# Kernel tuning notes

Hardware: AMD Instinct MI355X
Metric: run time of the kernel (lower is better)

## Reference

```python
import jax, jax.numpy as jnp
import numpy as np

COMMITMENT_COST = 0.25

def _conv(x, w, stride, pad):
    return jax.lax.conv_general_dilated(
        x, w, window_strides=(stride, stride),
        padding=((pad, pad), (pad, pad)),
        dimension_numbers=("NCHW", "OIHW", "NCHW"))

def _gelu(x):
    return jax.nn.gelu(x, approximate=False)

def setup_inputs() -> dict:
    key = jax.random.key(0)
    ks = jax.random.split(key, 9)
    def w(k, shape):
        fan_in = shape[1] * shape[2] * shape[3]
        return jax.random.normal(k, shape, jnp.float32) / jnp.sqrt(fan_in)
    return {
        "x": jax.random.normal(ks[0], (32, 3, 256, 256), jnp.float32),
        "enc_w1": w(ks[1], (64, 3, 5, 5)),
        "enc_w2": w(ks[2], (64, 64, 5, 5)),
        "enc_w3": w(ks[3], (64, 64, 2, 2)),
        "dec_w1": w(ks[4], (512, 64, 2, 2)),
        "dec_w2": w(ks[5], (256, 512, 2, 2)),
        "dec_w3": w(ks[6], (256, 256, 2, 2)),
        "codes": jax.random.normal(ks[7], (24, 64), jnp.float32),
        "ema_count": jax.random.uniform(ks[8], (24,), jnp.float32) + 0.1,
    }

def reference(x, enc_w1, enc_w2, enc_w3, dec_w1, dec_w2, dec_w3, codes, ema_count):
    # ---- encoder: 256 -> 128 -> 64 -> 63, channels 3 -> 64 ----
    z = _conv(x, enc_w1, 2, 2)
    z = _gelu(z)
    z = _conv(z, enc_w2, 2, 2)
    z = _gelu(z)
    z = _conv(z, enc_w3, 1, 0)          # [B, 64, 63, 63]

    # ---- VQ codebook (EMA variant: commitment loss only) ----
    B, C, H, W = z.shape
    zf = jnp.transpose(z, (0, 2, 3, 1)).reshape(-1, C)          # [N, C]
    # squared L2 distances to each code
    d = (jnp.sum(zf * zf, axis=1, keepdims=True)
         - 2.0 * zf @ codes.T
         + jnp.sum(codes * codes, axis=1))                       # [N, K]
    idx = jnp.argmin(d, axis=1)                                  # [N]
    zq = codes[idx].reshape(B, H, W, C).transpose(0, 3, 1, 2)    # [B, C, H, W]

    vq_loss = COMMITMENT_COST * jnp.mean(
        (jax.lax.stop_gradient(zq) - z) ** 2)
    # straight-through estimator
    z_hat = z + jax.lax.stop_gradient(zq - z)

    # code probabilities from EMA cluster counts, gathered per position
    probs = ema_count / jnp.sum(ema_count)                       # [K]
    z_probs = probs[idx].reshape(B, H, W)                        # [B, H, W]

    # ---- decoder: 63 -> 64 -> 63 -> 64, channels 64 -> 512 -> 256 -> 256 ----
    y = _conv(z_hat, dec_w1, 1, 1)
    y = _gelu(y)
    y = _conv(y, dec_w2, 1, 0)
    y = _gelu(y)
    x_hat = _conv(y, dec_w3, 1, 1)      # [B, 256, 64, 64]

    return (x_hat, z_probs, vq_loss)
```

## Files before the change

kernel.cpp:

```cpp
#include <hip/hip_runtime.h>
#include <hip/hip_bf16.h>


#define DEV_INLINE __device__ __forceinline__

typedef __attribute__((ext_vector_type(8))) short bf16x8;
typedef __attribute__((ext_vector_type(4))) float f32x4;

#define GLL16(g, l) __builtin_amdgcn_global_load_lds(                      \
    (const __attribute__((address_space(1))) void*)(g),                    \
    (__attribute__((address_space(3))) void*)(l), 16, 0, 0)

DEV_INLINE float gelu_exact(float v) {
    return 0.5f * v * (1.0f + erff(v * 0.70710678118654752440f));
}

__global__ void wtf_k(const float* __restrict__ w, float* __restrict__ wt,
                      int C, int total) {
    int t = blockIdx.x * 256 + threadIdx.x;
    if (t >= total) return;
    int oc = t & 63;
    int rest = t >> 6;
    int tap = rest % 25, c = rest / 25;
    wt[t] = w[(oc * C + c) * 25 + tap];
}

template<int C, int IH, int IW>
__global__ __launch_bounds__(256) void conv5s2_t(
    const float* __restrict__ xg,
    const float* __restrict__ wt,
    float* __restrict__ outg) {
    constexpr int OH = IH / 2, OW = IW / 2;
    __shared__ float xin[35 * 36];
    __shared__ float wl[1600];
    const int tid = threadIdx.x;
    const int n = blockIdx.z;
    const int OY0 = blockIdx.y * 16, OX0 = blockIdx.x * 16;
    const int IY0 = OY0 * 2 - 2, IX0 = OX0 * 2 - 2;
    const int og = tid & 3;
    const int pg = tid >> 2;
    const int py = (pg >> 3) * 2, px = (pg & 7) * 2;
    const int ry = py * 2, rx = px * 2;

    f32x4 a00 = {0,0,0,0}, a01 = a00, a02 = a00, a03 = a00;
    f32x4 a10 = a00, a11 = a00, a12 = a00, a13 = a00;
    f32x4 a20 = a00, a21 = a00, a22 = a00, a23 = a00;
    f32x4 a30 = a00, a31 = a00, a32 = a00, a33 = a00;

    const float* xn = xg + (size_t)n * C * IH * IW;
    for (int c = 0; c < C; ++c) {
        {
            const float4* wsrc = (const float4*)(wt + c * 1600);
            float4* wdst = (float4*)wl;
            wdst[tid] = wsrc[tid];
            if (tid < 144) wdst[256 + tid] = wsrc[256 + tid];
        }
        const float* zc = xn + (size_t)c * IH * IW;
        for (int i = tid; i < 1225; i += 256) {
            int r = i / 35, cl = i - r * 35;
            int iy = IY0 + r, ix = IX0 + cl;
            float v = 0.f;
            if ((unsigned)iy < (unsigned)IH && (unsigned)ix < (unsigned)IW)
                v = zc[(size_t)iy * IW + ix];
            xin[r * 36 + cl] = v;
        }
        __syncthreads();
#pragma unroll
        for (int ky = 0; ky < 5; ++ky) {
            const float* r0 = xin + (ry + ky) * 36 + rx;
            const float* r1 = r0 + 72;
#pragma unroll
            for (int kx = 0; kx < 5; ++kx) {
                const f32x4* wq = (const f32x4*)(wl + (ky * 5 + kx) * 64 + og * 16);
                f32x4 w0 = wq[0], w1 = wq[1], w2 = wq[2], w3 = wq[3];
                float xA = r0[kx], xB = r0[kx + 2];
                float xC = r1[kx], xD = r1[kx + 2];
                a00 += xA * w0; a01 += xA * w1; a02 += xA * w2; a03 += xA * w3;
                a10 += xB * w0; a11 += xB * w1; a12 += xB * w2; a13 += xB * w3;
                a20 += xC * w0; a21 += xC * w1; a22 += xC * w2; a23 += xC * w3;
                a30 += xD * w0; a31 += xD * w1; a32 += xD * w2; a33 += xD * w3;
            }
        }
        __syncthreads();
    }
    const int ocb = og * 16;
#define CSTORE(v, oy, ox, q) {                                                \
        float* o = outg + (((size_t)n * 64 + ocb + (q) * 4) * OH + (oy)) * OW \
                   + (ox);                                                    \
        o[0]               = gelu_exact((v).x);                               \
        o[(size_t)OH * OW]     = gelu_exact((v).y);                           \
        o[(size_t)2 * OH * OW] = gelu_exact((v).z);                           \
        o[(size_t)3 * OH * OW] = gelu_exact((v).w); }
    CSTORE(a00, OY0 + py,     OX0 + px,     0); CSTORE(a01, OY0 + py,     OX0 + px,     1);
    CSTORE(a02, OY0 + py,     OX0 + px,     2); CSTORE(a03, OY0 + py,     OX0 + px,     3);
    CSTORE(a10, OY0 + py,     OX0 + px + 1, 0); CSTORE(a11, OY0 + py,     OX0 + px + 1, 1);
    CSTORE(a12, OY0 + py,     OX0 + px + 1, 2); CSTORE(a13, OY0 + py,     OX0 + px + 1, 3);
    CSTORE(a20, OY0 + py + 1, OX0 + px,     0); CSTORE(a21, OY0 + py + 1, OX0 + px,     1);
    CSTORE(a22, OY0 + py + 1, OX0 + px,     2); CSTORE(a23, OY0 + py + 1, OX0 + px,     3);
    CSTORE(a30, OY0 + py + 1, OX0 + px + 1, 0); CSTORE(a31, OY0 + py + 1, OX0 + px + 1, 1);
    CSTORE(a32, OY0 + py + 1, OX0 + px + 1, 2); CSTORE(a33, OY0 + py + 1, OX0 + px + 1, 3);
#undef CSTORE
}

__global__ void conv3_k(const float* __restrict__ z2,
                        const float* __restrict__ w,
                        float* __restrict__ z) {
    __shared__ float wl[1024];
    const int oc0 = blockIdx.y * 4;
    for (int i = threadIdx.x; i < 1024; i += 256) {
        int j = i & 3, r = i >> 2;
        wl[i] = w[(oc0 + j) * 256 + r];
    }
    __syncthreads();
    const int s = blockIdx.x * 256 + threadIdx.x;
    if (s >= 3969) return;
    const int n = blockIdx.z;
    const int oy = s / 63, ox = s % 63;
    const float4* wv = (const float4*)wl;
    float a0 = 0.f, a1 = 0.f, a2 = 0.f, a3 = 0.f;
    const float* zn = z2 + n * 64 * 4096;
    for (int c = 0; c < 64; ++c) {
        const float* zc = zn + c * 4096;
#pragma unroll
        for (int tap = 0; tap < 4; ++tap) {
            int iy = oy + (tap >> 1), ix = ox + (tap & 1);
            float xv = zc[iy * 64 + ix];
            float4 wq = wv[c * 4 + tap];
            a0 += xv * wq.x; a1 += xv * wq.y; a2 += xv * wq.z; a3 += xv * wq.w;
        }
    }
    int obase = (n * 64 + oc0) * 3969 + s;
    z[obase]            = a0;
    z[obase + 3969]     = a1;
    z[obase + 2 * 3969] = a2;
    z[obase + 3 * 3969] = a3;
}

__global__ void vq_k(const float* __restrict__ z,
                     const float* __restrict__ codes,
                     const float* __restrict__ ema,
                     int* __restrict__ idxO,
                     float* __restrict__ zprobsO,
                     float* __restrict__ lossO) {
    __shared__ float cl[1536];
    __shared__ float cn[24];
    __shared__ float pr[24];
    for (int i = threadIdx.x; i < 1536; i += 256) cl[i] = codes[i];
    if (threadIdx.x < 24) pr[threadIdx.x] = ema[threadIdx.x];
    __syncthreads();
    if (threadIdx.x < 24) {
        float sm = 0.f;
        for (int c = 0; c < 64; ++c) { float v = cl[threadIdx.x * 64 + c]; sm += v * v; }
        cn[threadIdx.x] = sm;
    }
    __syncthreads();
    int t = blockIdx.x * 256 + threadIdx.x;
    float l = 0.f;
    if (t < 127008) {
        int b = t / 3969, s = t - b * 3969;
        const float* zp = z + (b * 64) * 3969 + s;
        float zv[64];
        float zn = 0.f;
#pragma unroll
        for (int c = 0; c < 64; ++c) { float v = zp[c * 3969]; zv[c] = v; zn += v * v; }
        float best = 1e30f; int bi = 0;
        for (int k = 0; k < 24; ++k) {
            float dot = 0.f;
#pragma unroll
            for (int c = 0; c < 64; ++c) dot += zv[c] * cl[k * 64 + c];
            float d = zn - 2.f * dot + cn[k];
            if (d < best) { best = d; bi = k; }
        }
        idxO[t] = bi;
        float psum = 0.f;
        for (int k = 0; k < 24; ++k) psum += pr[k];
        zprobsO[t] = pr[bi] / psum;
        for (int c = 0; c < 64; ++c) { float dd = cl[bi * 64 + c] - zv[c]; l += dd * dd; }
    }
    for (int off = 32; off; off >>= 1) l += __shfl_down(l, off, 64);
    if ((threadIdx.x & 63) == 0) atomicAdd(lossO, l);
}

__global__ void dtab_k(const float* __restrict__ codes,
                       const float* __restrict__ w1,
                       float* __restrict__ D) {
    int t = blockIdx.x * 256 + threadIdx.x;
    if (t >= 24 * 4 * 512) return;
    int oc = t & 511, tap = (t >> 9) & 3, k = t >> 11;
    float acc = 0.f;
    for (int c = 0; c < 64; ++c)
        acc += codes[k * 64 + c] * w1[oc * 256 + c * 4 + tap];
    D[t] = acc;
}

__global__ void wt_k(const float* __restrict__ w, __hip_bfloat16* __restrict__ wT,
                     int cl2, int total) {
    int t = blockIdx.x * 256 + threadIdx.x;
    if (t >= total) return;
    int c = t & ((1 << cl2) - 1);
    int tap = (t >> cl2) & 3;
    int oc = t >> (cl2 + 2);
    wT[t] = __float2bfloat16(w[((oc << cl2) + c) * 4 + tap]);
}

__global__ void dec1_k(const int* __restrict__ idx,
                       const float* __restrict__ D,
                       __hip_bfloat16* __restrict__ y1) {
    const int pos = blockIdx.x;
    const int n = pos >> 12, rem = pos & 4095;
    const int iy = rem >> 6, ix = rem & 63;
    const int* idn = idx + n * 3969;
    const int t = threadIdx.x;
    float ax = 0.f, ay = 0.f;
#pragma unroll
    for (int tap = 0; tap < 4; ++tap) {
        int py = iy - 1 + (tap >> 1), px = ix - 1 + (tap & 1);
        if ((unsigned)py < 63u && (unsigned)px < 63u) {
            int k = idn[py * 63 + px];
            float2 v = ((const float2*)(D + (k * 4 + tap) * 512))[t];
            ax += v.x; ay += v.y;
        }
    }
    __hip_bfloat162 o;
    o.x = __float2bfloat16(gelu_exact(ax));
    o.y = __float2bfloat16(gelu_exact(ay));
    ((__hip_bfloat162*)(y1 + (size_t)pos * 512))[t] = o;
}

__global__ __launch_bounds__(256) void dec2_mfma(
    const __hip_bfloat16* __restrict__ y1,
    const __hip_bfloat16* __restrict__ wT,
    const __hip_bfloat16* __restrict__ zp,
    __hip_bfloat16* __restrict__ y2)
{
    __shared__ __hip_bfloat16 As[128 * 32];
    __shared__ __hip_bfloat16 Bs[128 * 32];
    const int tid = threadIdx.x;
    const int wave = tid >> 6, lane = tid & 63;
    const int quad = lane >> 4, l15 = lane & 15;
    const int m0 = blockIdx.x * 128;
    const int oc0 = blockIdx.y * 128;
    const int sub = tid & 3;

    const char* pA[2];
    const char* pB[2];
#pragma unroll
    for (int j = 0; j < 2; ++j) {
        int slot = j * 64 + (tid >> 2);
        int pp = m0 + slot;
        if (pp < 127008) {
            int n = pp / 3969; int r = pp - n * 3969;
            int oy = r / 63;  int ox = r - oy * 63;
            pA[j] = (const char*)y1 + (size_t)((n * 64 + oy) * 64 + ox) * 1024 + sub * 16;
        } else {
            pA[j] = (const char*)zp;
        }
        pB[j] = (const char*)wT + (size_t)(oc0 + slot) * 4096 + sub * 16;
    }
    char* ldsA[2] = {(char*)As + wave * 1024, (char*)As + 4096 + wave * 1024};
    char* ldsB[2] = {(char*)Bs + wave * 1024, (char*)Bs + 4096 + wave * 1024};

    f32x4 acc[4][4] = {};
    const int wm = (wave & 1) * 64;
    const int wn = (wave >> 1) * 64;

#pragma unroll
    for (int tap = 0; tap < 4; ++tap) {
        const int toff = ((tap >> 1) * 64 + (tap & 1)) * 1024;
        for (int kk = 0; kk < 16; ++kk) {
            const int cb = kk * 64;
            GLL16(pA[0] + toff + cb, ldsA[0]);
            GLL16(pA[1] + toff + cb, ldsA[1]);
            GLL16(pB[0] + tap * 1024 + cb, ldsB[0]);
            GLL16(pB[1] + tap * 1024 + cb, ldsB[1]);
            __syncthreads();
            bf16x8 af[4], bf[4];
#pragma unroll
            for (int mi = 0; mi < 4; ++mi)
                af[mi] = *(const bf16x8*)((const char*)As + (wm + mi * 16 + l15) * 64 + quad * 16);
#pragma unroll
            for (int ni = 0; ni < 4; ++ni)
                bf[ni] = *(const bf16x8*)((const char*)Bs + (wn + ni * 16 + l15) * 64 + quad * 16);
#pragma unroll
            for (int mi = 0; mi < 4; ++mi)
#pragma unroll
                for (int ni = 0; ni < 4; ++ni)
                    acc[mi][ni] = __builtin_amdgcn_mfma_f32_16x16x32_bf16(
                        af[mi], bf[ni], acc[mi][ni], 0, 0, 0);
            __syncthreads();
        }
    }
#pragma unroll
    for (int mi = 0; mi < 4; ++mi)
#pragma unroll
        for (int r = 0; r < 4; ++r) {
            int pos = m0 + wm + mi * 16 + quad * 4 + r;
            if (pos < 127008) {
#pragma unroll
                for (int ni = 0; ni < 4; ++ni) {
                    int oc = oc0 + wn + ni * 16 + l15;
                    y2[(size_t)pos * 256 + oc] =
                        __float2bfloat16(gelu_exact(acc[mi][ni][r]));
                }
            }
        }
}

__global__ __launch_bounds__(256) void dec3_mfma(
    const __hip_bfloat16* __restrict__ y2,
    const __hip_bfloat16* __restrict__ wT,
    const __hip_bfloat16* __restrict__ zp,
    float* __restrict__ out)
{
    __shared__ __hip_bfloat16 As[128 * 32];
    __shared__ __hip_bfloat16 Bs[128 * 32];
    const int tid = threadIdx.x;
    const int wave = tid >> 6, lane = tid & 63;
    const int quad = lane >> 4, l15 = lane & 15;
    const int p0 = blockIdx.x * 128;
    const int oc0 = blockIdx.y * 128;
    const int sub = tid & 3;

    const char* pW[2];
    const char* pP[4][2];
#pragma unroll
    for (int j = 0; j < 2; ++j) {
        int slot = j * 64 + (tid >> 2);
        pW[j] = (const char*)wT + (size_t)(oc0 + slot) * 2048 + sub * 16;
        int pp = p0 + slot;
        int n = pp >> 12, rem = pp & 4095;
        int OY = rem >> 6, OX = rem & 63;
#pragma unroll
        for (int tap = 0; tap < 4; ++tap) {
            int iy = OY - 1 + (tap >> 1), ix = OX - 1 + (tap & 1);
            if ((unsigned)iy < 63u && (unsigned)ix < 63u)
                pP[tap][j] = (const char*)y2 + (size_t)(n * 3969 + iy * 63 + ix) * 512 + sub * 16;
            else
                pP[tap][j] = (const char*)zp;
        }
    }
    char* ldsA[2] = {(char*)As + wave * 1024, (char*)As + 4096 + wave * 1024};
    char* ldsB[2] = {(char*)Bs + wave * 1024, (char*)Bs + 4096 + wave * 1024};

    f32x4 acc[4][4] = {};
    const int wm = (wave & 1) * 64;
    const int wn = (wave >> 1) * 64;

#pragma unroll
    for (int tap = 0; tap < 4; ++tap) {
        for (int kk = 0; kk < 8; ++kk) {
            const int cb = kk * 64;
            GLL16(pW[0] + tap * 512 + cb, ldsA[0]);
            GLL16(pW[1] + tap * 512 + cb, ldsA[1]);
            GLL16(pP[tap][0] + cb, ldsB[0]);
            GLL16(pP[tap][1] + cb, ldsB[1]);
            __syncthreads();
            bf16x8 af[4], bf[4];
#pragma unroll
            for (int mi = 0; mi < 4; ++mi)
                af[mi] = *(const bf16x8*)((const char*)As + (wm + mi * 16 + l15) * 64 + quad * 16);
#pragma unroll
            for (int ni = 0; ni < 4; ++ni)
                bf[ni] = *(const bf16x8*)((const char*)Bs + (wn + ni * 16 + l15) * 64 + quad * 16);
#pragma unroll
            for (int mi = 0; mi < 4; ++mi)
#pragma unroll
                for (int ni = 0; ni < 4; ++ni)
                    acc[mi][ni] = __builtin_amdgcn_mfma_f32_16x16x32_bf16(
                        af[mi], bf[ni], acc[mi][ni], 0, 0, 0);
            __syncthreads();
        }
    }
    const int n = p0 >> 12;
    const int posLocal0 = (p0 & 4095) + wn;
#pragma unroll
    for (int mi = 0; mi < 4; ++mi)
#pragma unroll
        for (int r = 0; r < 4; ++r) {
            int oc = oc0 + wm + mi * 16 + quad * 4 + r;
            float* orow = out + ((size_t)(n * 256 + oc) << 12);
#pragma unroll
            for (int ni = 0; ni < 4; ++ni)
                orow[posLocal0 + ni * 16 + l15] = acc[mi][ni][r];
        }
}

__global__ void loss_k(const float* __restrict__ lossO, float* __restrict__ out) {
    out[0] = 0.25f * lossO[0] / 8128512.0f;
}

extern "C" void kernel_launch(void* const* d_in, const int* in_sizes, int n_in,
                              void* d_out, int out_size, void* d_ws, size_t ws_size,
                              hipStream_t stream) {
    const float* x     = (const float*)d_in[0];
    const float* ew1   = (const float*)d_in[1];
    const float* ew2   = (const float*)d_in[2];
    const float* ew3   = (const float*)d_in[3];
    const float* dw1   = (const float*)d_in[4];
    const float* dw2   = (const float*)d_in[5];
    const float* dw3   = (const float*)d_in[6];
    const float* codes = (const float*)d_in[7];
    const float* ema   = (const float*)d_in[8];
    float* out = (float*)d_out;

    char* ws = (char*)d_ws;
    float* z1   = (float*)(ws + 0);
    float* z2   = (float*)(ws + 134217728);
    float* z    = (float*)(ws + 167772160);
    int*   idx  = (int*)  (ws + 200286208);
    float* loss = (float*)(ws + 200794240);
    __hip_bfloat16* zp  = (__hip_bfloat16*)(ws + 200794496);
    float* D    = (float*)(ws + 200864128);
    __hip_bfloat16* wT2 = (__hip_bfloat16*)(ws + 201650560);
    __hip_bfloat16* wT3 = (__hip_bfloat16*)(ws + 202699136);
    float* wt2f = (float*)(ws + 201650560);
    float* wt1f = (float*)(ws + 202699136);
    __hip_bfloat16* y1  = (__hip_bfloat16*)(ws + 0);
    __hip_bfloat16* y2  = (__hip_bfloat16*)(ws + 134217728);

    hipMemsetAsync(loss, 0, 4, stream);
    hipMemsetAsync(zp, 0, 69632, stream);

    wtf_k<<<dim3(19), 256, 0, stream>>>(ew1, wt1f, 3, 4800);
    wtf_k<<<dim3(400), 256, 0, stream>>>(ew2, wt2f, 64, 102400);
    conv5s2_t<3, 256, 256><<<dim3(8, 8, 32), 256, 0, stream>>>(x, wt1f, z1);
    conv5s2_t<64, 128, 128><<<dim3(4, 4, 32), 256, 0, stream>>>(z1, wt2f, z2);
    conv3_k<<<dim3(16, 16, 32), 256, 0, stream>>>(z2, ew3, z);
    vq_k<<<dim3(497), 256, 0, stream>>>(z, codes, ema, idx, out + 33554432, loss);
    dtab_k<<<dim3(192), 256, 0, stream>>>(codes, dw1, D);
    wt_k<<<dim3(2048), 256, 0, stream>>>(dw2, wT2, 9, 524288);
    wt_k<<<dim3(1024), 256, 0, stream>>>(dw3, wT3, 8, 262144);
    dec1_k<<<dim3(131072), 256, 0, stream>>>(idx, D, y1);
    dec2_mfma<<<dim3(993, 2), 256, 0, stream>>>(y1, wT2, zp, y2);
    dec3_mfma<<<dim3(1024, 2), 256, 0, stream>>>(y2, wT3, zp, out);
    loss_k<<<1, 1, 0, stream>>>(loss, out + 33681440);
}
```

Baseline: 1.230 ms.

## Replace second encoder conv with smaller-tile, triple-buffered, weight-pipelined FP32 kernel

Adds a new 5x5 stride-2 convolution kernel for the second encoder layer. It uses 8x16 output tiles, so twice as many blocks run, and stages input rows in a triple-buffered shared layout split by even and odd columns. Weights are prefetched per kernel row in a ping-pong register scheme, and outputs are written as vector stores. The goal is more parallelism, overlap of global loads with FMA work, and fewer scalar shared and global accesses. In exchange, halo overhead per tile is higher and register pressure rises under a launch bound of 3 waves.

```diff
diff --git a/kernel.cpp b/kernel.cpp
--- a/kernel.cpp
+++ b/kernel.cpp
@@ -102,6 +102,142 @@
 #undef CSTORE
 }
 
+template<int C, int IH, int IW>
+__global__ __launch_bounds__(256, 3) void conv5s2_q(
+    const float* __restrict__ xg,
+    const float* __restrict__ wt,
+    float* __restrict__ outg) {
+    constexpr int OH = IH / 2, OW = IW / 2;
+    __shared__ float xp[3 * 760];
+    const int tid = threadIdx.x;
+    const int n = blockIdx.z;
+    const int OY0 = blockIdx.y * 8, OX0 = blockIdx.x * 16;
+    const int IY0 = OY0 * 2 - 2, IX0 = OX0 * 2 - 2;
+    const int og = tid & 15;
+    const int pg = tid >> 4;
+    const int py = (pg >> 2) * 2;
+    const int px = (pg & 3) * 4;
+    const int ry = py * 2;
+
+    int sG0, sG1, sG2, sL0, sL1, sL2;
+    bool sIn0, sIn1, sIn2;
+    const bool sWr2 = (tid < 172);
+    {
+        int s = tid;       int r = s / 36, cl = s - r * 36;
+        int iy = IY0 + r,  ix = IX0 + cl;
+        sIn0 = ((unsigned)iy < (unsigned)IH) && ((unsigned)ix < (unsigned)IW);
+        sG0 = sIn0 ? (iy * IW + ix) : 0;
+        sL0 = (cl & 1) * 380 + r * 20 + (cl >> 1);
+        s = tid + 256;     r = s / 36; cl = s - r * 36;
+        iy = IY0 + r;      ix = IX0 + cl;
+        sIn1 = ((unsigned)iy < (unsigned)IH) && ((unsigned)ix < (unsigned)IW);
+        sG1 = sIn1 ? (iy * IW + ix) : 0;
+        sL1 = (cl & 1) * 380 + r * 20 + (cl >> 1);
+        s = tid + 512;     r = s / 36; cl = s - r * 36;
+        iy = IY0 + r;      ix = IX0 + cl;
+        sIn2 = sWr2 && ((unsigned)iy < (unsigned)IH) &&
+               ((unsigned)ix < (unsigned)IW);
+        sG2 = sIn2 ? (iy * IW + ix) : 0;
+        sL2 = sWr2 ? ((cl & 1) * 380 + r * 20 + (cl >> 1)) : 0;
+    }
+
+    const float* xn = xg + (size_t)n * C * IH * IW;
+    const float* wtb = wt + og * 4;
+
+    float xr0, xr1, xr2;
+#define XLOAD(cc) { const float* zc = xn + (size_t)(cc) * IH * IW;          \
+        xr0 = sIn0 ? zc[sG0] : 0.f;                                         \
+        xr1 = sIn1 ? zc[sG1] : 0.f;                                         \
+        xr2 = sIn2 ? zc[sG2] : 0.f; }
+#define XWRITE(bw) { float* xw = xp + (bw) * 760;                           \
+        xw[sL0] = xr0; xw[sL1] = xr1; if (sWr2) xw[sL2] = xr2; }
+
+    f32x4 a00 = {0,0,0,0}, a01 = a00, a02 = a00, a03 = a00;
+    f32x4 a10 = a00, a11 = a00, a12 = a00, a13 = a00;
+    f32x4 wA0, wA1, wA2, wA3, wA4, wB0, wB1, wB2, wB3, wB4;
+#define WLOAD(P, cc, ky) {                                                  \
+        const float* wp = wtb + (size_t)(cc) * 1600 + (ky) * 320;           \
+        P##0 = *(const f32x4*)(wp);       P##1 = *(const f32x4*)(wp + 64);  \
+        P##2 = *(const f32x4*)(wp + 128); P##3 = *(const f32x4*)(wp + 192); \
+        P##4 = *(const f32x4*)(wp + 256); }
+
+#define PICK8(Qa, Qb, i) ((i) < 4 ? (Qa)[(i) & 3] : (Qb)[(i) & 3])
+#define XVV(R, kx, jj) (((kx) & 1)                                          \
+        ? PICK8(O##R##0, O##R##1, (jj) + ((kx) >> 1))                       \
+        : PICK8(E##R##0, E##R##1, (jj) + ((kx) >> 1)))
+#define KYBODY(ky, W) {                                                     \
+        const float* e0 = xb + (ry + (ky)) * 20 + px;                       \
+        const float* o0 = e0 + 380;                                         \
+        const f32x4 E00 = *(const f32x4*)e0;                                \
+        const f32x4 E01 = *(const f32x4*)(e0 + 4);                          \
+        const f32x4 O00 = *(const f32x4*)o0;                                \
+        const f32x4 O01 = *(const f32x4*)(o0 + 4);                          \
+        const f32x4 E10 = *(const f32x4*)(e0 + 40);                         \
+        const f32x4 E11 = *(const f32x4*)(e0 + 44);                         \
+        const f32x4 O10 = *(const f32x4*)(o0 + 40);                         \
+        const f32x4 O11 = *(const f32x4*)(o0 + 44);                         \
+        _Pragma("unroll")                                                   \
+        for (int kx = 0; kx < 5; ++kx) {                                    \
+            const f32x4 wv = (kx == 0) ? W##0 : (kx == 1) ? W##1            \
+                           : (kx == 2) ? W##2 : (kx == 3) ? W##3 : W##4;    \
+            float xA = XVV(0, kx, 0), xB = XVV(0, kx, 1);                   \
+            float xC = XVV(0, kx, 2), xD = XVV(0, kx, 3);                   \
+            float xE = XVV(1, kx, 0), xF = XVV(1, kx, 1);                   \
+            float xG = XVV(1, kx, 2), xH = XVV(1, kx, 3);                   \
+            a00 += xA * wv; a01 += xB * wv; a02 += xC * wv; a03 += xD * wv; \
+            a10 += xE * wv; a11 += xF * wv; a12 += xG * wv; a13 += xH * wv; \
+        } }
+
+    XLOAD(0)
+    XWRITE(0)
+    XLOAD(1)
+    WLOAD(wA, 0, 0)
+
+    int br = 0;
+    for (int c = 0; c < C; ++c) {
+        const int bw = (br + 1 >= 3) ? br + 1 - 3 : br + 1;
+        XWRITE(bw)
+        if (c + 2 < C) XLOAD(c + 2)
+        __syncthreads();
+        const float* xb = xp + br * 760;
+        const int cn = (c + 1 < C) ? (c + 1) : c;
+        if ((c & 1) == 0) {
+            WLOAD(wB, c, 1)  KYBODY(0, wA)
+            WLOAD(wA, c, 2)  KYBODY(1, wB)
+            WLOAD(wB, c, 3)  KYBODY(2, wA)
+            WLOAD(wA, c, 4)  KYBODY(3, wB)
+            WLOAD(wB, cn, 0) KYBODY(4, wA)
+        } else {
+            WLOAD(wA, c, 1)  KYBODY(0, wB)
+            WLOAD(wB, c, 2)  KYBODY(1, wA)
+            WLOAD(wA, c, 3)  KYBODY(2, wB)
+            WLOAD(wB, c, 4)  KYBODY(3, wA)
+            WLOAD(wA, cn, 0) KYBODY(4, wB)
+        }
+        br = bw;
+    }
+#undef KYBODY
+#undef XVV
+#undef PICK8
+#undef WLOAD
+#undef XWRITE
+#undef XLOAD
+
+    const size_t HW = (size_t)OH * OW;
+#pragma unroll
+    for (int j = 0; j < 4; ++j) {
+        float* o = outg + ((size_t)n * 64 + og * 4 + j) * HW
+                   + (size_t)(OY0 + py) * OW + (OX0 + px);
+        f32x4 t0, t1;
+        t0[0] = gelu_exact(a00[j]); t0[1] = gelu_exact(a01[j]);
+        t0[2] = gelu_exact(a02[j]); t0[3] = gelu_exact(a03[j]);
+        t1[0] = gelu_exact(a10[j]); t1[1] = gelu_exact(a11[j]);
+        t1[2] = gelu_exact(a12[j]); t1[3] = gelu_exact(a13[j]);
+        *(f32x4*)o = t0;
+        *(f32x4*)(o + OW) = t1;
+    }
+}
+
 __global__ void conv3_k(const float* __restrict__ z2,
                         const float* __restrict__ w,
                         float* __restrict__ z) {
@@ -424,7 +560,7 @@
     wtf_k<<<dim3(19), 256, 0, stream>>>(ew1, wt1f, 3, 4800);
     wtf_k<<<dim3(400), 256, 0, stream>>>(ew2, wt2f, 64, 102400);
     conv5s2_t<3, 256, 256><<<dim3(8, 8, 32), 256, 0, stream>>>(x, wt1f, z1);
-    conv5s2_t<64, 128, 128><<<dim3(4, 4, 32), 256, 0, stream>>>(z1, wt2f, z2);
+    conv5s2_q<64, 128, 128><<<dim3(4, 8, 32), 256, 0, stream>>>(z1, wt2f, z2);
     conv3_k<<<dim3(16, 16, 32), 256, 0, stream>>>(z2, ew3, z);
     vq_k<<<dim3(497), 256, 0, stream>>>(z, codes, ema, idx, out + 33554432, loss);
     dtab_k<<<dim3(192), 256, 0, stream>>>(codes, dw1, D);
```

Measured after the change: 2.456 ms. 99.7% more time.
